# Kernel optimization log

Hardware: AMD Instinct MI355X
Metric: run time of the kernel (lower is better)

The kernel has to match this reference:

```python
import jax, jax.numpy as jnp
import numpy as np

B, N, FIN, FOUT = 8, 4096, 64, 64
NEG_SLOPE = 0.01  # torch LeakyReLU default


def setup_inputs() -> dict:
    key = jax.random.key(0)
    k1, k2, k3, k4, k5 = jax.random.split(key, 5)
    inp = jax.random.normal(k1, (B, N, FIN), dtype=jnp.float32)
    adj = jax.random.randint(k2, (N, N), 0, 2, dtype=jnp.int32)
    W_w = jax.random.normal(k3, (FOUT, FIN), dtype=jnp.float32) * (1.0 / np.sqrt(FIN))
    W_b = jax.random.normal(k4, (FOUT,), dtype=jnp.float32) * 0.01
    a = jax.random.normal(k5, (2 * FOUT, N), dtype=jnp.float32) * (1.414 / np.sqrt(2 * FOUT + N))
    return {"inp": inp, "adj": adj, "W_w": W_w, "W_b": W_b, "a": a}


def reference(inp, adj, W_w, W_b, a):
    # h = W(inp); h[:, 0, :] = 0
    h = jnp.einsum('bnf,of->bno', inp, W_w) + W_b          # [B, N, F]
    h = h.at[:, 0, :].set(0.0)

    # Original loop: for i in 1..N-1:
    #   ac = a[:, i]  (shape [2F, 1])
    #   index = where(adj[1:, i] > 0)  -> 0-based, used to index h directly (bug preserved)
    #   s_i = h[:, i, :] @ ac[:F] + sum_j h[:, index, :] @ ac[F:]   (scalar per batch)
    #   attention[:, i, :] = s_i broadcast over all columns
    # Empty-index case equals the general case since an empty neighbor sum is 0.
    mask = (adj[1:, :] > 0).astype(h.dtype)                # [N-1, N]
    neigh = jnp.einsum('ji,bjf->bif', mask, h[:, :N - 1, :])  # [B, N, F]
    s = (jnp.einsum('bif,fi->bi', h, a[:FOUT]) +
         jnp.einsum('bif,fi->bi', neigh, a[FOUT:]))        # [B, N]
    s = s.at[:, 0].set(0.0)                                # attention row 0 stays zero

    # h_prime = attention @ h, with attention[b,i,j] = s[b,i] for all j
    hsum = h.sum(axis=1)                                   # [B, F]
    h_prime = s[:, :, None] * hsum[:, None, :]             # [B, N, F]
    return jnp.where(h_prime >= 0, h_prime, NEG_SLOPE * h_prime)
```

## Files before the change

### kernel.cpp

```cpp
#include <hip/hip_runtime.h>
#include <hip/hip_bf16.h>

#define NN 4096

typedef unsigned short u16;
typedef __attribute__((ext_vector_type(8))) short short8;
typedef __attribute__((ext_vector_type(4))) float f32x4;
typedef __attribute__((ext_vector_type(4))) unsigned short u16x4;
typedef __attribute__((ext_vector_type(8))) unsigned short u16x8;
typedef __attribute__((ext_vector_type(4))) int i32x4;

typedef const void __attribute__((address_space(1)))* gas_t;
typedef void __attribute__((address_space(3)))* las_t;

__device__ __forceinline__ u16 f2bf(float x) {
  unsigned u = __float_as_uint(x);
  return (u16)((u + 0x7FFFu + ((u >> 16) & 1)) >> 16);
}

__global__ __launch_bounds__(256) void k_prep(const int* __restrict__ adj, const float* __restrict__ inp,
                                              const float* __restrict__ Ww, const float* __restrict__ Wb,
                                              const float* __restrict__ a, u16* __restrict__ maskT,
                                              u16* __restrict__ h2t, float* __restrict__ p1,
                                              float* __restrict__ hpart, float* __restrict__ s) {
  __shared__ __align__(16) char Lraw[33792];
  __shared__ float wsum[4][64];
  const int bid = blockIdx.x;
  const int t = threadIdx.x;

  if (bid < 1024) {
    u16* tile = (u16*)Lraw;
    const int i0 = (bid & 31) * 128, j0 = (bid >> 5) * 128;
    const int jr = t >> 5;
    const int il = t & 31;
#pragma unroll
    for (int pass = 0; pass < 16; ++pass) {
      const int jl = pass * 8 + jr;
      const int j = j0 + jl;
      u16 q[4] = {0, 0, 0, 0};
      if (j < NN - 1) {
        i32x4 av = *reinterpret_cast<const i32x4*>(&adj[(size_t)(j + 1) * NN + i0 + il * 4]);
        q[0] = av.x > 0 ? 0x3F80 : 0;
        q[1] = av.y > 0 ? 0x3F80 : 0;
        q[2] = av.z > 0 ? 0x3F80 : 0;
        q[3] = av.w > 0 ? 0x3F80 : 0;
      }
      const int pb = il ^ (jl >> 2);
      *reinterpret_cast<u16x4*>(&tile[jl * 132 + pb * 4]) = *reinterpret_cast<u16x4*>(q);
    }
    __syncthreads();
#pragma unroll
    for (int pass = 0; pass < 16; ++pass) {
      const int ir = pass * 8 + jr;
      const int ci = ir >> 2, io = ir & 3;
      u16 o[4];
#pragma unroll
      for (int d = 0; d < 4; ++d) {
        const int r = il * 4 + d;
        o[d] = tile[r * 132 + ((ci ^ il) << 2) + io];
      }
      *reinterpret_cast<u16x4*>(&maskT[(size_t)(i0 + ir) * NN + j0 + il * 4]) =
          *reinterpret_cast<u16x4*>(o);
    }
    return;
  }

  u16* lA = (u16*)Lraw;
  u16* lW = (u16*)(Lraw + 16384);
  const int hb = bid - 1024;
  const int lane = t & 63, w = t >> 6;
  const int b = hb >> 5;
  const size_t row0 = (size_t)hb * 128;
  if (t < 128) s[hb * 128 + t] = 0.f;
  {
    const int o = t >> 2, k0 = (t & 3) * 16;
    const float* src = &Ww[o * 64 + k0];
    u16 tmp[16];
#pragma unroll
    for (int e = 0; e < 16; ++e) tmp[e] = f2bf(src[e]);
    const int swz = (o & 7) * 8;
#pragma unroll
    for (int v = 0; v < 2; ++v)
      *reinterpret_cast<u16x8*>(&lW[o * 64 + ((k0 + v * 8) ^ swz)]) = *reinterpret_cast<u16x8*>(&tmp[v * 8]);
  }
  {
    const int r = t >> 1, k0 = (t & 1) * 32;
    const float* src = &inp[(row0 + r) * 64 + k0];
    u16 tmp[32];
#pragma unroll
    for (int e = 0; e < 32; ++e) tmp[e] = f2bf(src[e]);
    const int swz = (r & 7) * 8;
#pragma unroll
    for (int v = 0; v < 4; ++v)
      *reinterpret_cast<u16x8*>(&lA[r * 64 + ((k0 + v * 8) ^ swz)]) = *reinterpret_cast<u16x8*>(&tmp[v * 8]);
  }
  __syncthreads();
  f32x4 acc[2][4] = {};
#pragma unroll
  for (int ks = 0; ks < 2; ++ks) {
    const int kk = ks * 32 + (lane >> 4) * 8;
    short8 af[2], bf[4];
#pragma unroll
    for (int m = 0; m < 2; ++m) {
      const int row = w * 32 + m * 16 + (lane & 15);
      af[m] = *reinterpret_cast<const short8*>(&lA[row * 64 + (kk ^ ((row & 7) * 8))]);
    }
#pragma unroll
    for (int n = 0; n < 4; ++n) {
      const int o = n * 16 + (lane & 15);
      bf[n] = *reinterpret_cast<const short8*>(&lW[o * 64 + (kk ^ ((o & 7) * 8))]);
    }
#pragma unroll
    for (int m = 0; m < 2; ++m)
#pragma unroll
      for (int n = 0; n < 4; ++n)
        acc[m][n] = __builtin_amdgcn_mfma_f32_16x16x32_bf16(af[m], bf[n], acc[m][n], 0, 0, 0);
  }
  const int f0 = lane & 15;
  const int rsub = (lane >> 4) * 4;
  float wb[4];
#pragma unroll
  for (int n = 0; n < 4; ++n) wb[n] = Wb[n * 16 + f0];
  const int nloc_base = (hb & 31) * 128;
  float ps[4] = {0.f, 0.f, 0.f, 0.f};
#pragma unroll
  for (int m = 0; m < 2; ++m) {
    const int rl = w * 32 + m * 16 + rsub;
    float vz[4][4];
#pragma unroll
    for (int n = 0; n < 4; ++n) {
      u16 hb4[4];
#pragma unroll
      for (int r = 0; r < 4; ++r) {
        float v = acc[m][n][r] + wb[n];
        if (nloc_base + rl + r == 0) v = 0.f;
        vz[n][r] = v;
        hb4[r] = f2bf(v);
        ps[n] += v;
      }
      *reinterpret_cast<u16x4*>(&h2t[(size_t)(b * 64 + n * 16 + f0) * NN + nloc_base + rl]) =
          *reinterpret_cast<u16x4*>(&hb4[0]);
    }
#pragma unroll
    for (int r = 0; r < 4; ++r) {
      const int ig = nloc_base + rl + r;
      float pv = 0.f;
#pragma unroll
      for (int n = 0; n < 4; ++n) pv += vz[n][r] * a[(size_t)(n * 16 + f0) * NN + ig];
      pv += __shfl_xor(pv, 1);
      pv += __shfl_xor(pv, 2);
      pv += __shfl_xor(pv, 4);
      pv += __shfl_xor(pv, 8);
      if (f0 == 0) p1[(size_t)b * NN + ig] = pv;
    }
  }
#pragma unroll
  for (int n = 0; n < 4; ++n) {
    float v = ps[n];
    v += __shfl_xor(v, 16);
    v += __shfl_xor(v, 32);
    if (lane < 16) wsum[w][n * 16 + f0] = v;
  }
  __syncthreads();
  if (t < 64) hpart[hb * 64 + t] = wsum[0][t] + wsum[1][t] + wsum[2][t] + wsum[3][t];
}

__global__ __launch_bounds__(256, 2) void k_gemm(const u16* __restrict__ A, const u16* __restrict__ Bm,
                                                 const float* __restrict__ a, float* __restrict__ s) {
  __shared__ __align__(16) u16 lA0[128 * 64], lA1[128 * 64];
  __shared__ __align__(16) u16 lB0[128 * 64], lB1[128 * 64];
  const int sid = blockIdx.x;
  const int wgid = (sid & 7) * 64 + (sid >> 3);
  const int c0 = (wgid & 3) * 128;
  const int i0 = ((wgid >> 2) & 31) * 128;
  const int z = wgid >> 7;
  const int t = threadIdx.x, lane = t & 63, w = t >> 6;
  const int wr = w >> 1, wc = w & 1;

  const int srow = lane >> 3;
  const int sk = ((lane & 7) ^ srow) * 8;
  const size_t kbase = (size_t)z * 1024;
  const u16* gA = A + (size_t)(i0 + w * 32 + srow) * NN + kbase + sk;
  const u16* gB = Bm + (size_t)(c0 + w * 32 + srow) * NN + kbase + sk;

#define STAGE_K(dstA, dstB, kt)                                                              \
  do {                                                                                       \
    _Pragma("unroll") for (int c = 0; c < 4; ++c) {                                          \
      __builtin_amdgcn_global_load_lds((gas_t)(gA + (size_t)(8 * c) * NN + (kt)),            \
                                       (las_t)((dstA) + (w * 32 + 8 * c) * 128 + lane * 16), \
                                       16, 0, 0);                                            \
      __builtin_amdgcn_global_load_lds((gas_t)(gB + (size_t)(8 * c) * NN + (kt)),            \
                                       (las_t)((dstB) + (w * 32 + 8 * c) * 128 + lane * 16), \
                                       16, 0, 0);                                            \
    }                                                                                        \
  } while (0)

  f32x4 acc[4][4] = {};
  asm volatile("" ::: "memory");
  STAGE_K((char*)lA0, (char*)lB0, 0);
#pragma unroll 1
  for (int it = 0; it < 16; ++it) {
    char* nA = (it & 1) ? (char*)lA0 : (char*)lA1;
    char* nB = (it & 1) ? (char*)lB0 : (char*)lB1;
    if (it < 15) {
      STAGE_K(nA, nB, (it + 1) * 64);
      asm volatile("s_waitcnt vmcnt(8)" ::: "memory");
    } else {
      asm volatile("s_waitcnt vmcnt(0)" ::: "memory");
    }
    __builtin_amdgcn_s_barrier();
    asm volatile("" ::: "memory");
    const u16* cA = (it & 1) ? lA1 : lA0;
    const u16* cB = (it & 1) ? lB1 : lB0;
#pragma unroll
    for (int ks = 0; ks < 2; ++ks) {
      const int kb = ks * 4 + (lane >> 4);
      short8 af[4], bfr[4];
#pragma unroll
      for (int m = 0; m < 4; ++m) {
        const int row = wr * 64 + m * 16 + (lane & 15);
        af[m] = *reinterpret_cast<const short8*>(&cA[row * 64 + ((kb ^ (row & 7)) * 8)]);
      }
#pragma unroll
      for (int n = 0; n < 4; ++n) {
        const int row = wc * 64 + n * 16 + (lane & 15);
        bfr[n] = *reinterpret_cast<const short8*>(&cB[row * 64 + ((kb ^ (row & 7)) * 8)]);
      }
#pragma unroll
      for (int m = 0; m < 4; ++m)
#pragma unroll
        for (int n = 0; n < 4; ++n)
          acc[m][n] = __builtin_amdgcn_mfma_f32_16x16x32_bf16(af[m], bfr[n], acc[m][n], 0, 0, 0);
    }
    asm volatile("" ::: "memory");
    __builtin_amdgcn_s_barrier();
  }
#undef STAGE_K
  const int b = (c0 >> 7) * 2 + wc;
  const int f0 = lane & 15, rsub = (lane >> 4) * 4;
  float pp[4][4];
#pragma unroll
  for (int m = 0; m < 4; ++m) {
    const int irow = i0 + wr * 64 + m * 16 + rsub;
#pragma unroll
    for (int r = 0; r < 4; ++r) pp[m][r] = 0.f;
#pragma unroll
    for (int n = 0; n < 4; ++n) {
      f32x4 a2v = *reinterpret_cast<const f32x4*>(&a[(size_t)(64 + n * 16 + f0) * NN + irow]);
#pragma unroll
      for (int r = 0; r < 4; ++r) pp[m][r] += acc[m][n][r] * a2v[r];
    }
  }
#pragma unroll
  for (int m = 0; m < 4; ++m)
#pragma unroll
    for (int r = 0; r < 4; ++r) {
      float v = pp[m][r];
      v += __shfl_xor(v, 1);
      v += __shfl_xor(v, 2);
      v += __shfl_xor(v, 4);
      v += __shfl_xor(v, 8);
      pp[m][r] = v;
    }
  if (f0 == 0) {
    const int irow = i0 + wr * 64 + rsub;
#pragma unroll
    for (int m = 0; m < 4; ++m)
#pragma unroll
      for (int r = 0; r < 4; ++r)
        atomicAdd(&s[(size_t)b * NN + irow + m * 16 + r], pp[m][r]);
  }
}

__global__ __launch_bounds__(256) void k_final(const float* __restrict__ p1, const float* __restrict__ sg,
                                               const float* __restrict__ hpart, float* __restrict__ out) {
  __shared__ float hp[4][64];
  __shared__ float hs[64], sv[64];
  const int b = blockIdx.x >> 6;
  const int i0 = (blockIdx.x & 63) * 64;
  const int t = threadIdx.x;
  {
    const int f = t & 63, g = t >> 6;
    float acc = 0.f;
#pragma unroll
    for (int sl = 0; sl < 8; ++sl) acc += hpart[(size_t)(b * 32 + g * 8 + sl) * 64 + f];
    hp[g][f] = acc;
  }
  __syncthreads();
  if (t < 64) {
    hs[t] = hp[0][t] + hp[1][t] + hp[2][t] + hp[3][t];
    const int i = i0 + t;
    sv[t] = (i == 0) ? 0.f : (p1[(size_t)b * NN + i] + sg[(size_t)b * NN + i]);
  }
  __syncthreads();
  const int fq = (t & 15) * 4, ir = t >> 4;
#pragma unroll
  for (int pass = 0; pass < 4; ++pass) {
    const int ii = pass * 16 + ir;
    const float svi = sv[ii];
    f32x4 o;
#pragma unroll
    for (int k = 0; k < 4; ++k) {
      float val = svi * hs[fq + k];
      o[k] = (val >= 0.f) ? val : 0.01f * val;
    }
    *reinterpret_cast<f32x4*>(&out[((size_t)b * NN + i0 + ii) * 64 + fq]) = o;
  }
}

extern "C" void kernel_launch(void* const* d_in, const int* in_sizes, int n_in,
                              void* d_out, int out_size, void* d_ws, size_t ws_size,
                              hipStream_t stream) {
  const float* inp = (const float*)d_in[0];
  const int* adj = (const int*)d_in[1];
  const float* Ww = (const float*)d_in[2];
  const float* Wb = (const float*)d_in[3];
  const float* a = (const float*)d_in[4];
  float* out = (float*)d_out;
  char* ws = (char*)d_ws;

  float* s = (float*)ws;
  float* hpart = (float*)(ws + 131072);
  float* p1 = (float*)(ws + 196608);
  u16* maskT = (u16*)(ws + 524288);
  u16* h2t = (u16*)(ws + 524288 + 33554432);

  hipLaunchKernelGGL(k_prep, dim3(1280), dim3(256), 0, stream, adj, inp, Ww, Wb, a,
                     maskT, h2t, p1, hpart, s);
  hipLaunchKernelGGL(k_gemm, dim3(512), dim3(256), 0, stream, maskT, h2t, a, s);
  hipLaunchKernelGGL(k_final, dim3(512), dim3(256), 0, stream, p1, s, hpart, out);
}
```

Before: 153.6 us.

## Pack adjacency mask as bits and expand to bf16 via LDS lookup in GEMM

The prep kernel no longer writes a transposed bf16 mask matrix. It now packs adj>0 into 32-bit words, one bit per j, laid out by j-word and i, which cuts that workspace write from 32 MB to 2 MB and shrinks the A-tile reads in the GEMM by the same factor. The GEMM loads one packed word per row into LDS and expands it to bf16 MFMA fragments through a 16-entry lookup table. This frees LDS, so launch bounds rise to 4 blocks per CU. The cost is extra ALU and LDS work to decode each A fragment, and the bit-order mapping must match the MFMA k layout exactly.

```diff
diff --git a/kernel.cpp b/kernel.cpp
--- a/kernel.cpp
+++ b/kernel.cpp
@@ -20,47 +20,42 @@
 
 __global__ __launch_bounds__(256) void k_prep(const int* __restrict__ adj, const float* __restrict__ inp,
                                               const float* __restrict__ Ww, const float* __restrict__ Wb,
-                                              const float* __restrict__ a, u16* __restrict__ maskT,
+                                              const float* __restrict__ a, unsigned* __restrict__ AbitsT,
                                               u16* __restrict__ h2t, float* __restrict__ p1,
                                               float* __restrict__ hpart, float* __restrict__ s) {
-  __shared__ __align__(16) char Lraw[33792];
+  __shared__ __align__(16) char Lraw[24576];
   __shared__ float wsum[4][64];
   const int bid = blockIdx.x;
   const int t = threadIdx.x;
 
   if (bid < 1024) {
-    u16* tile = (u16*)Lraw;
     const int i0 = (bid & 31) * 128, j0 = (bid >> 5) * 128;
-    const int jr = t >> 5;
-    const int il = t & 31;
-#pragma unroll
-    for (int pass = 0; pass < 16; ++pass) {
-      const int jl = pass * 8 + jr;
-      const int j = j0 + jl;
-      u16 q[4] = {0, 0, 0, 0};
-      if (j < NN - 1) {
-        i32x4 av = *reinterpret_cast<const i32x4*>(&adj[(size_t)(j + 1) * NN + i0 + il * 4]);
-        q[0] = av.x > 0 ? 0x3F80 : 0;
-        q[1] = av.y > 0 ? 0x3F80 : 0;
-        q[2] = av.z > 0 ? 0x3F80 : 0;
-        q[3] = av.w > 0 ? 0x3F80 : 0;
-      }
-      const int pb = il ^ (jl >> 2);
-      *reinterpret_cast<u16x4*>(&tile[jl * 132 + pb * 4]) = *reinterpret_cast<u16x4*>(q);
-    }
-    __syncthreads();
-#pragma unroll
-    for (int pass = 0; pass < 16; ++pass) {
-      const int ir = pass * 8 + jr;
-      const int ci = ir >> 2, io = ir & 3;
-      u16 o[4];
-#pragma unroll
-      for (int d = 0; d < 4; ++d) {
-        const int r = il * 4 + d;
-        o[d] = tile[r * 132 + ((ci ^ il) << 2) + io];
-      }
-      *reinterpret_cast<u16x4*>(&maskT[(size_t)(i0 + ir) * NN + j0 + il * 4]) =
-          *reinterpret_cast<u16x4*>(o);
+    const int jr = t >> 5, il = t & 31;
+    i32x4 av[16];
+#pragma unroll
+    for (int p = 0; p < 16; ++p) {
+      const int j = j0 + jr * 16 + p;
+      if (j < NN - 1)
+        av[p] = *reinterpret_cast<const i32x4*>(&adj[(size_t)(j + 1) * NN + i0 + il * 4]);
+      else
+        av[p] = i32x4{0, 0, 0, 0};
+    }
+    unsigned accb[4] = {0, 0, 0, 0};
+#pragma unroll
+    for (int p = 0; p < 16; ++p)
+#pragma unroll
+      for (int d = 0; d < 4; ++d)
+        accb[d] |= (av[p][d] > 0 ? 1u : 0u) << p;
+    unsigned wout[4];
+#pragma unroll
+    for (int d = 0; d < 4; ++d) {
+      unsigned part = (unsigned)__shfl_xor((int)accb[d], 32);
+      wout[d] = accb[d] | (part << 16);
+    }
+    if ((jr & 1) == 0) {
+      const int jw = (j0 >> 5) + (jr >> 1);
+      *reinterpret_cast<i32x4*>(&AbitsT[(size_t)jw * NN + i0 + il * 4]) =
+          *reinterpret_cast<i32x4*>(wout);
     }
     return;
   }
@@ -165,10 +160,11 @@
   if (t < 64) hpart[hb * 64 + t] = wsum[0][t] + wsum[1][t] + wsum[2][t] + wsum[3][t];
 }
 
-__global__ __launch_bounds__(256, 2) void k_gemm(const u16* __restrict__ A, const u16* __restrict__ Bm,
+__global__ __launch_bounds__(256, 4) void k_gemm(const unsigned* __restrict__ Ab, const u16* __restrict__ Bm,
                                                  const float* __restrict__ a, float* __restrict__ s) {
-  __shared__ __align__(16) u16 lA0[128 * 64], lA1[128 * 64];
   __shared__ __align__(16) u16 lB0[128 * 64], lB1[128 * 64];
+  __shared__ __align__(16) unsigned lAb0[256], lAb1[256];
+  __shared__ __align__(16) u16 lut[16][4];
   const int sid = blockIdx.x;
   const int wgid = (sid & 7) * 64 + (sid >> 3);
   const int c0 = (wgid & 3) * 128;
@@ -176,54 +172,62 @@
   const int z = wgid >> 7;
   const int t = threadIdx.x, lane = t & 63, w = t >> 6;
   const int wr = w >> 1, wc = w & 1;
+  if (t < 16) {
+    lut[t][0] = (t & 1) ? 0x3F80 : 0;
+    lut[t][1] = (t & 2) ? 0x3F80 : 0;
+    lut[t][2] = (t & 4) ? 0x3F80 : 0;
+    lut[t][3] = (t & 8) ? 0x3F80 : 0;
+  }
 
   const int srow = lane >> 3;
   const int sk = ((lane & 7) ^ srow) * 8;
   const size_t kbase = (size_t)z * 1024;
-  const u16* gA = A + (size_t)(i0 + w * 32 + srow) * NN + kbase + sk;
   const u16* gB = Bm + (size_t)(c0 + w * 32 + srow) * NN + kbase + sk;
-
-#define STAGE_K(dstA, dstB, kt)                                                              \
+  const unsigned* gAb = Ab + (size_t)(z * 32 + (lane >> 5)) * NN + i0 + (lane & 31) * 4;
+
+#define STAGE_K(dstB, dstA, it_)                                                             \
   do {                                                                                       \
+    __builtin_amdgcn_global_load_lds((gas_t)(gAb + (size_t)(it_) * 2 * NN),                  \
+                                     (las_t)((char*)(dstA) + lane * 16), 16, 0, 0);          \
     _Pragma("unroll") for (int c = 0; c < 4; ++c) {                                          \
-      __builtin_amdgcn_global_load_lds((gas_t)(gA + (size_t)(8 * c) * NN + (kt)),            \
-                                       (las_t)((dstA) + (w * 32 + 8 * c) * 128 + lane * 16), \
-                                       16, 0, 0);                                            \
-      __builtin_amdgcn_global_load_lds((gas_t)(gB + (size_t)(8 * c) * NN + (kt)),            \
-                                       (las_t)((dstB) + (w * 32 + 8 * c) * 128 + lane * 16), \
+      __builtin_amdgcn_global_load_lds((gas_t)(gB + (size_t)(8 * c) * NN + (it_) * 64),      \
+                                       (las_t)((char*)(dstB) + (w * 32 + 8 * c) * 128 + lane * 16), \
                                        16, 0, 0);                                            \
     }                                                                                        \
   } while (0)
 
   f32x4 acc[4][4] = {};
   asm volatile("" ::: "memory");
-  STAGE_K((char*)lA0, (char*)lB0, 0);
+  STAGE_K(lB0, lAb0, 0);
 #pragma unroll 1
   for (int it = 0; it < 16; ++it) {
-    char* nA = (it & 1) ? (char*)lA0 : (char*)lA1;
-    char* nB = (it & 1) ? (char*)lB0 : (char*)lB1;
     if (it < 15) {
-      STAGE_K(nA, nB, (it + 1) * 64);
-      asm volatile("s_waitcnt vmcnt(8)" ::: "memory");
+      if (it & 1) STAGE_K(lB0, lAb0, it + 1); else STAGE_K(lB1, lAb1, it + 1);
+      asm volatile("s_waitcnt vmcnt(5)" ::: "memory");
     } else {
       asm volatile("s_waitcnt vmcnt(0)" ::: "memory");
     }
     __builtin_amdgcn_s_barrier();
     asm volatile("" ::: "memory");
-    const u16* cA = (it & 1) ? lA1 : lA0;
     const u16* cB = (it & 1) ? lB1 : lB0;
+    const unsigned* cAb = (it & 1) ? lAb1 : lAb0;
+    const int q = lane >> 4;
 #pragma unroll
     for (int ks = 0; ks < 2; ++ks) {
-      const int kb = ks * 4 + (lane >> 4);
       short8 af[4], bfr[4];
 #pragma unroll
       for (int m = 0; m < 4; ++m) {
-        const int row = wr * 64 + m * 16 + (lane & 15);
-        af[m] = *reinterpret_cast<const short8*>(&cA[row * 64 + ((kb ^ (row & 7)) * 8)]);
+        const unsigned wrd = cAb[ks * 128 + wr * 64 + m * 16 + (lane & 15)];
+        const unsigned b8 = (wrd >> (q * 8)) & 0xFFu;
+        union { unsigned long long qq[2]; short8 s8; } u;
+        u.qq[0] = *reinterpret_cast<const unsigned long long*>(&lut[b8 & 15][0]);
+        u.qq[1] = *reinterpret_cast<const unsigned long long*>(&lut[b8 >> 4][0]);
+        af[m] = u.s8;
       }
 #pragma unroll
       for (int n = 0; n < 4; ++n) {
         const int row = wc * 64 + n * 16 + (lane & 15);
+        const int kb = ks * 4 + q;
         bfr[n] = *reinterpret_cast<const short8*>(&cB[row * 64 + ((kb ^ (row & 7)) * 8)]);
       }
 #pragma unroll
@@ -322,11 +326,11 @@
   float* s = (float*)ws;
   float* hpart = (float*)(ws + 131072);
   float* p1 = (float*)(ws + 196608);
-  u16* maskT = (u16*)(ws + 524288);
-  u16* h2t = (u16*)(ws + 524288 + 33554432);
+  unsigned* AbitsT = (unsigned*)(ws + 524288);
+  u16* h2t = (u16*)(ws + 524288 + 2097152);
 
   hipLaunchKernelGGL(k_prep, dim3(1280), dim3(256), 0, stream, adj, inp, Ww, Wb, a,
-                     maskT, h2t, p1, hpart, s);
-  hipLaunchKernelGGL(k_gemm, dim3(512), dim3(256), 0, stream, maskT, h2t, a, s);
+                     AbitsT, h2t, p1, hpart, s);
+  hipLaunchKernelGGL(k_gemm, dim3(512), dim3(256), 0, stream, AbitsT, h2t, a, s);
   hipLaunchKernelGGL(k_final, dim3(512), dim3(256), 0, stream, p1, s, hpart, out);
 }
```

After: 142.6 us. 1.08x faster.
